# Kernel tuning notes

Measured on AMD Instinct MI355X. Metric: run time of the kernel, lower is better.

The kernel has to match this reference:

```python
import jax, jax.numpy as jnp
import numpy as np

N = 200000   # active voxels
C = 128      # in_channels == out_channels -> identity downsample
K = 27       # 3x3x3 kernel offsets
EPS = 1e-5


def setup_inputs() -> dict:
    key = jax.random.key(0)
    ks = jax.random.split(key, 4)
    x = jax.random.normal(ks[0], (N, C), jnp.float32)
    nbr = jax.random.randint(ks[1], (N, K), 0, N, jnp.int32)
    W1 = jax.random.normal(ks[2], (K, C, C), jnp.float32) * 0.05
    W2 = jax.random.normal(ks[3], (K, C, C), jnp.float32) * 0.05
    g1 = jnp.ones((C,), jnp.float32); b1 = jnp.zeros((C,), jnp.float32)
    g2 = jnp.ones((C,), jnp.float32); b2 = jnp.zeros((C,), jnp.float32)
    return {"x": x, "nbr": nbr, "W1": W1, "g1": g1, "b1": b1,
            "W2": W2, "g2": g2, "b2": b2}


def _sparse_conv(x, nbr, W):
    # gather-matmul-scatter sparse conv: out[i] = sum_k W[k]^T x[nbr[i,k]]
    # scan over the K=27 kernel offsets to avoid materializing [N,K,C].
    def body(acc, kn):
        Wk, nk = kn                               # [C,C], [N]
        return acc + jnp.take(x, nk, axis=0) @ Wk, None
    acc0 = jnp.zeros((x.shape[0], W.shape[2]), x.dtype)
    out, _ = jax.lax.scan(body, acc0, (W, nbr.T))
    return out


def _bn(x, g, b):
    # training-mode batch norm over the point dimension
    m = jnp.mean(x, axis=0)
    v = jnp.var(x, axis=0)
    return (x - m) * jax.lax.rsqrt(v + EPS) * g + b


def reference(x, nbr, W1, g1, b1, W2, g2, b2):
    out = jax.nn.relu(_bn(_sparse_conv(x, nbr, W1), g1, b1))
    out = _bn(_sparse_conv(out, nbr, W2), g2, b2)
    # downsample is identity (in_channels == out_channels, stride == 1)
    return jax.nn.relu(out + x)
```

## Files before the change

kernel.cpp:

```cpp
#include <hip/hip_runtime.h>
#include <hip/hip_bf16.h>
#include <stdint.h>

#define C_DIM 128
#define K_DIM 27

typedef __attribute__((ext_vector_type(8))) short short8;
typedef __attribute__((ext_vector_type(4))) float f32x4;
typedef __attribute__((ext_vector_type(4))) unsigned short ushort4v;

#define FENCE() asm volatile("" ::: "memory")
#define VMCNT0() asm volatile("s_waitcnt vmcnt(0)" ::: "memory")
#define LGKM0() asm volatile("s_waitcnt lgkmcnt(0)" ::: "memory")
#define BAR() __builtin_amdgcn_s_barrier()

__device__ __forceinline__ unsigned short f2bf(float f) {
  unsigned int u = __builtin_bit_cast(unsigned int, f);
  u += 0x7fffu + ((u >> 16) & 1u);
  return (unsigned short)(u >> 16);
}
__device__ __forceinline__ float bf2f(unsigned short h) {
  unsigned int u = ((unsigned int)h) << 16;
  return __builtin_bit_cast(float, u);
}

__device__ __forceinline__ void async_copy16(const void* gsrc, void* ldst) {
  __builtin_amdgcn_global_load_lds(
      (const __attribute__((address_space(1))) unsigned int*)gsrc,
      (__attribute__((address_space(3))) unsigned int*)ldst, 16, 0, 0);
}

__global__ __launch_bounds__(256) void prep_kernel(
    const float* __restrict__ W1, const float* __restrict__ W2,
    unsigned short* __restrict__ Wt1, unsigned short* __restrict__ Wt2,
    float* __restrict__ stats, int stats_n) {
  int idx = blockIdx.x * 256 + threadIdx.x;
  const int total = K_DIM * C_DIM * C_DIM;
  if (idx < total) {
    int k = idx >> 14;
    int r = idx & 16383;
    int co = r >> 7;
    int gpos = (r >> 3) & 15;
    int e = r & 7;
    int gg = gpos ^ (co & 7);
    int ci = gg * 8 + e;
    int src = (k * C_DIM + ci) * C_DIM + co;
    Wt1[idx] = f2bf(W1[src]);
    Wt2[idx] = f2bf(W2[src]);
  }
  if (idx < stats_n) stats[idx] = 0.f;
}

__global__ __launch_bounds__(256) void cvt_x_kernel(
    const float* __restrict__ x, unsigned short* __restrict__ xb, int total4) {
  int i = blockIdx.x * 256 + threadIdx.x;
  if (i >= total4) return;
  f32x4 v = ((const f32x4*)x)[i];
  ushort4v u;
#pragma unroll
  for (int j = 0; j < 4; ++j) u[j] = f2bf(v[j]);
  ((ushort4v*)xb)[i] = u;
}

template<int OUT_IS_F32>
__global__ __launch_bounds__(512, 1) void conv_kernel(
    const unsigned short* __restrict__ xb, const int* __restrict__ nbr,
    const unsigned short* __restrict__ Wt, void* __restrict__ out_v,
    float* __restrict__ stats, int N) {
  extern __shared__ __align__(16) char smem[];
  unsigned short* Wbuf = (unsigned short*)smem;
  unsigned short* Abuf = (unsigned short*)(smem + 65536);
  int* idx_lds = (int*)(smem + 131072);
  float* s_sum = (float*)(smem + 131072 + 13824);
  float* s_ssum = s_sum + C_DIM;

  const int tid = threadIdx.x;
  const int wave = tid >> 6, lane = tid & 63;
  const int lr = lane & 15, lg = lane >> 4;
  const int rg = wave >> 1, cg = wave & 1;
  const int row0 = blockIdx.x * 128;

  if (tid < C_DIM) { s_sum[tid] = 0.f; s_ssum[tid] = 0.f; }

  for (int i = tid; i < 128 * K_DIM; i += 512) {
    int r = i / K_DIM;
    int k = i - r * K_DIM;
    int rr = row0 + r; if (rr >= N) rr = N - 1;
    idx_lds[i] = nbr[(size_t)rr * K_DIM + k];
  }
  __syncthreads();

  auto stage_a = [&](const int (&gi)[4], int buf) {
    unsigned short* dstb = Abuf + buf * 16384 + wave * 2048;
#pragma unroll
    for (int c = 0; c < 4; ++c) {
      const int rloc = wave * 16 + c * 4 + lg;
      const unsigned short* src =
          xb + (size_t)gi[c] * C_DIM + ((lr ^ (rloc & 7)) << 3);
      async_copy16(src, dstb + c * 512);
    }
  };
  auto stage_w = [&](int k, int buf) {
    const unsigned short* src = Wt + (size_t)k * 16384 + wave * 2048 + lane * 8;
    unsigned short* dstb = Wbuf + buf * 16384 + wave * 2048;
#pragma unroll
    for (int c = 0; c < 4; ++c)
      async_copy16(src + c * 512, dstb + c * 512);
  };
  auto read_gi = [&](int k, int (&gi)[4]) {
#pragma unroll
    for (int c = 0; c < 4; ++c)
      gi[c] = idx_lds[(wave * 16 + c * 4 + lg) * K_DIM + k];
  };

  int gi[4];
  read_gi(0, gi);
  stage_a(gi, 0);
  stage_w(0, 0);
  read_gi(1, gi);
  f32x4 acc[2][4] = {};
  LGKM0();
  VMCNT0();
  BAR();

  int cur = 0;
  for (int k = 0; k < K_DIM; ++k) {
    if (k + 1 < K_DIM) {
      stage_a(gi, cur ^ 1);
      stage_w(k + 1, cur ^ 1);
    }
    FENCE();
    { int kn = (k + 2 < K_DIM) ? k + 2 : K_DIM - 1; read_gi(kn, gi); }
    FENCE();
    const unsigned short* wb = Wbuf + cur * 16384;
    const unsigned short* ab = Abuf + cur * 16384;
    __builtin_amdgcn_s_setprio(1);
#pragma unroll
    for (int cs = 0; cs < 4; ++cs) {
      const int gq = cs * 4 + lg;
      const int sw = (gq ^ (lr & 7)) << 3;
      short8 a0 = *(const short8*)(ab + (rg * 32 + lr) * C_DIM + sw);
      short8 a1 = *(const short8*)(ab + (rg * 32 + 16 + lr) * C_DIM + sw);
#pragma unroll
      for (int ct = 0; ct < 4; ++ct) {
        const int co = cg * 64 + ct * 16 + lr;
        short8 b = *(const short8*)(wb + co * C_DIM + ((gq ^ (co & 7)) << 3));
        acc[0][ct] = __builtin_amdgcn_mfma_f32_16x16x32_bf16(a0, b, acc[0][ct], 0, 0, 0);
        acc[1][ct] = __builtin_amdgcn_mfma_f32_16x16x32_bf16(a1, b, acc[1][ct], 0, 0, 0);
      }
    }
    __builtin_amdgcn_s_setprio(0);
    LGKM0();
    VMCNT0();
    BAR();
    cur ^= 1;
  }

  float* ctile = (float*)Abuf;
  float ps[4] = {0.f, 0.f, 0.f, 0.f}, pss[4] = {0.f, 0.f, 0.f, 0.f};
  const int wr0 = rg * 32;
#pragma unroll
  for (int rt = 0; rt < 2; ++rt) {
#pragma unroll
    for (int j = 0; j < 4; ++j) {
      int lrow = wr0 + rt * 16 + lg * 4 + j;
      bool ok = (row0 + lrow) < N;
#pragma unroll
      for (int ct = 0; ct < 4; ++ct) {
        float v = acc[rt][ct][j];
        ctile[lrow * C_DIM + cg * 64 + ct * 16 + lr] = v;
        if (ok) { ps[ct] += v; pss[ct] += v * v; }
      }
    }
  }
#pragma unroll
  for (int ct = 0; ct < 4; ++ct) {
    ps[ct]  += __shfl_xor(ps[ct], 16, 64);
    ps[ct]  += __shfl_xor(ps[ct], 32, 64);
    pss[ct] += __shfl_xor(pss[ct], 16, 64);
    pss[ct] += __shfl_xor(pss[ct], 32, 64);
    if (lg == 0) {
      int col = cg * 64 + ct * 16 + lr;
      atomicAdd(&s_sum[col], ps[ct]);
      atomicAdd(&s_ssum[col], pss[ct]);
    }
  }
  __syncthreads();
  if (tid < C_DIM) {
    atomicAdd(&stats[tid], s_sum[tid]);
    atomicAdd(&stats[C_DIM + tid], s_ssum[tid]);
  }
  for (int i = tid; i < 4096; i += 512) {
    int row = i >> 5;
    int c4 = i & 31;
    int grow = row0 + row;
    if (grow >= N) continue;
    f32x4 v = ((const f32x4*)ctile)[i];
    if (OUT_IS_F32) {
      ((f32x4*)out_v)[(size_t)grow * 32 + c4] = v;
    } else {
      ushort4v u;
#pragma unroll
      for (int j = 0; j < 4; ++j) u[j] = f2bf(v[j]);
      ((ushort4v*)out_v)[(size_t)grow * 32 + c4] = u;
    }
  }
}

__global__ void finalize_kernel(const float* __restrict__ stats,
                                const float* __restrict__ g,
                                const float* __restrict__ b,
                                float* __restrict__ sshift, float invN) {
  int c = threadIdx.x;
  float mean = stats[c] * invN;
  float var = stats[128 + c] * invN - mean * mean;
  float sc = g[c] * rsqrtf(var + 1e-5f);
  sshift[c] = sc;
  sshift[128 + c] = b[c] - mean * sc;
}

__global__ __launch_bounds__(256) void apply_kernel(
    unsigned short* __restrict__ y, const float* __restrict__ ss, int total8) {
  int i = blockIdx.x * 256 + threadIdx.x;
  if (i >= total8) return;
  int cb = (i * 8) & 127;
  short8 u = ((short8*)y)[i];
#pragma unroll
  for (int j = 0; j < 8; ++j) {
    float f = bf2f((unsigned short)u[j]) * ss[cb + j] + ss[128 + cb + j];
    u[j] = (short)f2bf(fmaxf(f, 0.f));
  }
  ((short8*)y)[i] = u;
}

__global__ __launch_bounds__(256) void final_kernel(
    float* __restrict__ y2, const float* __restrict__ x,
    const float* __restrict__ ss, int total4) {
  int i = blockIdx.x * 256 + threadIdx.x;
  if (i >= total4) return;
  int cb = (i * 4) & 127;
  f32x4 v = ((const f32x4*)y2)[i];
  f32x4 xv = ((const f32x4*)x)[i];
#pragma unroll
  for (int j = 0; j < 4; ++j)
    v[j] = fmaxf(v[j] * ss[cb + j] + ss[128 + cb + j] + xv[j], 0.f);
  ((f32x4*)y2)[i] = v;
}

extern "C" void kernel_launch(void* const* d_in, const int* in_sizes, int n_in,
                              void* d_out, int out_size, void* d_ws, size_t ws_size,
                              hipStream_t stream) {
  const float* x  = (const float*)d_in[0];
  const int* nbr  = (const int*)d_in[1];
  const float* W1 = (const float*)d_in[2];
  const float* g1 = (const float*)d_in[3];
  const float* b1 = (const float*)d_in[4];
  const float* W2 = (const float*)d_in[5];
  const float* g2 = (const float*)d_in[6];
  const float* b2 = (const float*)d_in[7];
  float* out = (float*)d_out;

  const int N = in_sizes[0] / C_DIM;
  const int totalW = K_DIM * C_DIM * C_DIM;
  const int SMEM_BYTES = 65536 + 65536 + 13824 + 1024;

  char* ws = (char*)d_ws;
  size_t off = 0;
  auto alloc = [&](size_t bytes) {
    void* p = ws + off;
    off = (off + bytes + 255) & ~(size_t)255;
    return p;
  };
  unsigned short* Wt1 = (unsigned short*)alloc((size_t)totalW * 2);
  unsigned short* Wt2 = (unsigned short*)alloc((size_t)totalW * 2);
  float* stats = (float*)alloc(512 * 4);
  float* ss1   = (float*)alloc(256 * 4);
  float* ss2   = (float*)alloc(256 * 4);
  unsigned short* y1 = (unsigned short*)alloc((size_t)N * C_DIM * 2);
  unsigned short* xb_ws = (unsigned short*)alloc((size_t)N * C_DIM * 2);
  unsigned short* xb = (off <= ws_size) ? xb_ws : (unsigned short*)d_out;

  (void)hipFuncSetAttribute((const void*)conv_kernel<0>,
      hipFuncAttributeMaxDynamicSharedMemorySize, SMEM_BYTES);
  (void)hipFuncSetAttribute((const void*)conv_kernel<1>,
      hipFuncAttributeMaxDynamicSharedMemorySize, SMEM_BYTES);

  const int nblk = (N + 127) / 128;
  const float invN = 1.0f / (float)N;

  prep_kernel<<<(totalW + 255) / 256, 256, 0, stream>>>(W1, W2, Wt1, Wt2, stats, 512);

  {
    int t4 = N * C_DIM / 4;
    cvt_x_kernel<<<(t4 + 255) / 256, 256, 0, stream>>>(x, xb, t4);
  }

  conv_kernel<0><<<nblk, 512, SMEM_BYTES, stream>>>(xb, nbr, Wt1, y1, stats, N);
  finalize_kernel<<<1, 128, 0, stream>>>(stats, g1, b1, ss1, invN);

  {
    int t8 = N * C_DIM / 8;
    apply_kernel<<<(t8 + 255) / 256, 256, 0, stream>>>(y1, ss1, t8);
  }

  conv_kernel<1><<<nblk, 512, SMEM_BYTES, stream>>>(y1, nbr, Wt2, out, stats + 256, N);
  finalize_kernel<<<1, 128, 0, stream>>>(stats + 256, g2, b2, ss2, invN);

  {
    int t4 = N * C_DIM / 4;
    final_kernel<<<(t4 + 255) / 256, 256, 0, stream>>>(out, x, ss2, t4);
  }
}
```

Measured before the change: 666.3 us.

## Split conv K-loop into channel halves with 256-thread blocks for two blocks per CU

The conv kernel now pipelines over 54 half-channel phases (64 input channels each) instead of 27 full ones, which halves the LDS footprint so two 256-thread blocks can share a CU. Each wave now computes a 64x64 tile with 16 accumulators instead of 32x64, which raises MFMA work per LDS fragment load. The weight pre-layout is rearranged to match the half-split swizzle. The trade-off is more barriers and smaller async copies per phase, plus higher register pressure from the larger accumulator tile.

```diff
diff --git a/kernel.cpp b/kernel.cpp
--- a/kernel.cpp
+++ b/kernel.cpp
@@ -37,13 +37,12 @@
   int idx = blockIdx.x * 256 + threadIdx.x;
   const int total = K_DIM * C_DIM * C_DIM;
   if (idx < total) {
+    int e = idx & 7;
+    int s = (idx >> 3) & 7;
+    int co = (idx >> 6) & 127;
+    int h = (idx >> 13) & 1;
     int k = idx >> 14;
-    int r = idx & 16383;
-    int co = r >> 7;
-    int gpos = (r >> 3) & 15;
-    int e = r & 7;
-    int gg = gpos ^ (co & 7);
-    int ci = gg * 8 + e;
+    int ci = h * 64 + ((s ^ (co & 7)) << 3) + e;
     int src = (k * C_DIM + ci) * C_DIM + co;
     Wt1[idx] = f2bf(W1[src]);
     Wt2[idx] = f2bf(W2[src]);
@@ -63,15 +62,15 @@
 }
 
 template<int OUT_IS_F32>
-__global__ __launch_bounds__(512, 1) void conv_kernel(
+__global__ __launch_bounds__(256, 2) void conv_kernel(
     const unsigned short* __restrict__ xb, const int* __restrict__ nbr,
     const unsigned short* __restrict__ Wt, void* __restrict__ out_v,
     float* __restrict__ stats, int N) {
   extern __shared__ __align__(16) char smem[];
   unsigned short* Wbuf = (unsigned short*)smem;
-  unsigned short* Abuf = (unsigned short*)(smem + 65536);
-  int* idx_lds = (int*)(smem + 131072);
-  float* s_sum = (float*)(smem + 131072 + 13824);
+  unsigned short* Abuf = (unsigned short*)(smem + 32768);
+  int* idx_lds = (int*)(smem + 65536);
+  float* s_sum = (float*)(smem + 65536 + 13824);
   float* s_ssum = s_sum + C_DIM;
 
   const int tid = threadIdx.x;
@@ -82,7 +81,7 @@
 
   if (tid < C_DIM) { s_sum[tid] = 0.f; s_ssum[tid] = 0.f; }
 
-  for (int i = tid; i < 128 * K_DIM; i += 512) {
+  for (int i = tid; i < 128 * K_DIM; i += 256) {
     int r = i / K_DIM;
     int k = i - r * K_DIM;
     int rr = row0 + r; if (rr >= N) rr = N - 1;
@@ -90,80 +89,94 @@
   }
   __syncthreads();
 
-  auto stage_a = [&](const int (&gi)[4], int buf) {
-    unsigned short* dstb = Abuf + buf * 16384 + wave * 2048;
+  const int sr = lane >> 3, g = lane & 7;
+
+  auto stage_a = [&](const int (&gi)[4], int h, int buf) {
+    unsigned short* dst = Abuf + buf * 8192 + wave * 2048;
 #pragma unroll
     for (int c = 0; c < 4; ++c) {
-      const int rloc = wave * 16 + c * 4 + lg;
       const unsigned short* src =
-          xb + (size_t)gi[c] * C_DIM + ((lr ^ (rloc & 7)) << 3);
-      async_copy16(src, dstb + c * 512);
-    }
-  };
-  auto stage_w = [&](int k, int buf) {
-    const unsigned short* src = Wt + (size_t)k * 16384 + wave * 2048 + lane * 8;
-    unsigned short* dstb = Wbuf + buf * 16384 + wave * 2048;
+          xb + (size_t)gi[c] * C_DIM + h * 64 + ((g ^ (sr & 7)) << 3);
+      async_copy16(src, dst + c * 512);
+    }
+  };
+  auto stage_w = [&](int p, int buf) {
+    const unsigned short* src = Wt + (size_t)p * 8192 + wave * 2048 + lane * 8;
+    unsigned short* dst = Wbuf + buf * 8192 + wave * 2048;
 #pragma unroll
     for (int c = 0; c < 4; ++c)
-      async_copy16(src + c * 512, dstb + c * 512);
+      async_copy16(src + c * 512, dst + c * 512);
   };
   auto read_gi = [&](int k, int (&gi)[4]) {
 #pragma unroll
     for (int c = 0; c < 4; ++c)
-      gi[c] = idx_lds[(wave * 16 + c * 4 + lg) * K_DIM + k];
-  };
-
-  int gi[4];
-  read_gi(0, gi);
-  stage_a(gi, 0);
+      gi[c] = idx_lds[(wave * 32 + c * 8 + sr) * K_DIM + k];
+  };
+
+  f32x4 acc[4][4] = {};
+
+  auto compute = [&](int buf) {
+    const unsigned short* ab = Abuf + buf * 8192;
+    const unsigned short* wb = Wbuf + buf * 8192;
+    __builtin_amdgcn_s_setprio(1);
+#pragma unroll
+    for (int cs = 0; cs < 2; ++cs) {
+      const int slot = ((cs * 4 + lg) ^ (lr & 7)) << 3;
+      short8 a[4], b[4];
+#pragma unroll
+      for (int rt = 0; rt < 4; ++rt)
+        a[rt] = *(const short8*)(ab + (rg * 64 + rt * 16 + lr) * 64 + slot);
+#pragma unroll
+      for (int ct = 0; ct < 4; ++ct)
+        b[ct] = *(const short8*)(wb + (cg * 64 + ct * 16 + lr) * 64 + slot);
+#pragma unroll
+      for (int rt = 0; rt < 4; ++rt)
+#pragma unroll
+        for (int ct = 0; ct < 4; ++ct)
+          acc[rt][ct] = __builtin_amdgcn_mfma_f32_16x16x32_bf16(a[rt], b[ct], acc[rt][ct], 0, 0, 0);
+    }
+    __builtin_amdgcn_s_setprio(0);
+  };
+
+  int giC[4], giN[4];
+  read_gi(0, giC);
+  LGKM0();
+  stage_a(giC, 0, 0);
   stage_w(0, 0);
-  read_gi(1, gi);
-  f32x4 acc[2][4] = {};
   LGKM0();
   VMCNT0();
   BAR();
 
-  int cur = 0;
-  for (int k = 0; k < K_DIM; ++k) {
-    if (k + 1 < K_DIM) {
-      stage_a(gi, cur ^ 1);
-      stage_w(k + 1, cur ^ 1);
+  const int NP = K_DIM * 2;
+#pragma unroll 2
+  for (int p = 0; p < NP; ++p) {
+    const int k = p >> 1, h = p & 1, cur = p & 1;
+    if (p + 1 < NP) {
+      if (h == 0) {
+        stage_a(giC, 1, cur ^ 1);
+        stage_w(p + 1, cur ^ 1);
+        read_gi(k + 1 < K_DIM ? k + 1 : k, giN);
+      } else {
+        stage_a(giN, 0, cur ^ 1);
+        stage_w(p + 1, cur ^ 1);
+#pragma unroll
+        for (int c = 0; c < 4; ++c) giC[c] = giN[c];
+      }
     }
     FENCE();
-    { int kn = (k + 2 < K_DIM) ? k + 2 : K_DIM - 1; read_gi(kn, gi); }
-    FENCE();
-    const unsigned short* wb = Wbuf + cur * 16384;
-    const unsigned short* ab = Abuf + cur * 16384;
-    __builtin_amdgcn_s_setprio(1);
-#pragma unroll
-    for (int cs = 0; cs < 4; ++cs) {
-      const int gq = cs * 4 + lg;
-      const int sw = (gq ^ (lr & 7)) << 3;
-      short8 a0 = *(const short8*)(ab + (rg * 32 + lr) * C_DIM + sw);
-      short8 a1 = *(const short8*)(ab + (rg * 32 + 16 + lr) * C_DIM + sw);
-#pragma unroll
-      for (int ct = 0; ct < 4; ++ct) {
-        const int co = cg * 64 + ct * 16 + lr;
-        short8 b = *(const short8*)(wb + co * C_DIM + ((gq ^ (co & 7)) << 3));
-        acc[0][ct] = __builtin_amdgcn_mfma_f32_16x16x32_bf16(a0, b, acc[0][ct], 0, 0, 0);
-        acc[1][ct] = __builtin_amdgcn_mfma_f32_16x16x32_bf16(a1, b, acc[1][ct], 0, 0, 0);
-      }
-    }
-    __builtin_amdgcn_s_setprio(0);
+    compute(cur);
     LGKM0();
     VMCNT0();
     BAR();
-    cur ^= 1;
-  }
-
-  float* ctile = (float*)Abuf;
+  }
+
+  float* ctile = (float*)smem;
   float ps[4] = {0.f, 0.f, 0.f, 0.f}, pss[4] = {0.f, 0.f, 0.f, 0.f};
-  const int wr0 = rg * 32;
-#pragma unroll
-  for (int rt = 0; rt < 2; ++rt) {
+#pragma unroll
+  for (int rt = 0; rt < 4; ++rt) {
 #pragma unroll
     for (int j = 0; j < 4; ++j) {
-      int lrow = wr0 + rt * 16 + lg * 4 + j;
+      int lrow = rg * 64 + rt * 16 + lg * 4 + j;
       bool ok = (row0 + lrow) < N;
 #pragma unroll
       for (int ct = 0; ct < 4; ++ct) {
@@ -190,7 +203,7 @@
     atomicAdd(&stats[tid], s_sum[tid]);
     atomicAdd(&stats[C_DIM + tid], s_ssum[tid]);
   }
-  for (int i = tid; i < 4096; i += 512) {
+  for (int i = tid; i < 4096; i += 256) {
     int row = i >> 5;
     int c4 = i & 31;
     int grow = row0 + row;
@@ -262,7 +275,7 @@
 
   const int N = in_sizes[0] / C_DIM;
   const int totalW = K_DIM * C_DIM * C_DIM;
-  const int SMEM_BYTES = 65536 + 65536 + 13824 + 1024;
+  const int SMEM_BYTES = 65536 + 13824 + 1024;
 
   char* ws = (char*)d_ws;
   size_t off = 0;
@@ -295,7 +308,7 @@
     cvt_x_kernel<<<(t4 + 255) / 256, 256, 0, stream>>>(x, xb, t4);
   }
 
-  conv_kernel<0><<<nblk, 512, SMEM_BYTES, stream>>>(xb, nbr, Wt1, y1, stats, N);
+  conv_kernel<0><<<nblk, 256, SMEM_BYTES, stream>>>(xb, nbr, Wt1, y1, stats, N);
   finalize_kernel<<<1, 128, 0, stream>>>(stats, g1, b1, ss1, invN);
 
   {
@@ -303,7 +316,7 @@
     apply_kernel<<<(t8 + 255) / 256, 256, 0, stream>>>(y1, ss1, t8);
   }
 
-  conv_kernel<1><<<nblk, 512, SMEM_BYTES, stream>>>(y1, nbr, Wt2, out, stats + 256, N);
+  conv_kernel<1><<<nblk, 256, SMEM_BYTES, stream>>>(y1, nbr, Wt2, out, stats + 256, N);
   finalize_kernel<<<1, 128, 0, stream>>>(stats + 256, g2, b2, ss2, invN);
 
   {
```

Measured after the change: 609.0 us. -8.6%, faster.
